# Kernel tuning notes

Hardware: AMD Instinct MI355X
Metric: run time of the kernel (lower is better)

Reference implementation:

```python
import jax, jax.numpy as jnp
from jax import lax
import numpy as np

SCALE, K_UP = 2, 5


def conv2d(x, w, pad=0, dil=1):
    return lax.conv_general_dilated(x, w, (1, 1), [(pad, pad), (pad, pad)],
                                    rhs_dilation=(dil, dil),
                                    dimension_numbers=('NCHW', 'OIHW', 'NCHW'))


def cbr(x, w, g, b, pad=0, relu=True):
    # Conv (no bias) + BatchNorm (eval: running_mean=0, running_var=1, eps=1e-5) + optional ReLU
    x = conv2d(x, w, pad)
    x = x * (g / jnp.sqrt(1.0 + 1e-5))[None, :, None, None] + b[None, :, None, None]
    return jnp.maximum(x, 0.0) if relu else x


def resize_bilinear_ac(x, ho, wo):
    # bilinear interpolation, align_corners=True (matches F.interpolate)
    B, C, H, W = x.shape
    ys = jnp.linspace(0.0, H - 1.0, ho)
    xs = jnp.linspace(0.0, W - 1.0, wo)
    y0 = jnp.floor(ys).astype(jnp.int32); y1 = jnp.minimum(y0 + 1, H - 1)
    x0 = jnp.floor(xs).astype(jnp.int32); x1 = jnp.minimum(x0 + 1, W - 1)
    wy = (ys - y0).astype(x.dtype)
    wx = (xs - x0).astype(x.dtype)
    top = x[:, :, y0, :]
    bot = x[:, :, y1, :]
    v = top * (1.0 - wy)[None, None, :, None] + bot * wy[None, None, :, None]
    return v[:, :, :, x0] * (1.0 - wx) + v[:, :, :, x1] * wx


def setup_inputs() -> dict:
    key = jax.random.key(0)
    ks = jax.random.split(key, 10)
    B, CH, CL, H, W = 4, 256, 128, 64, 64
    CMID, CO, IC, KENC = 64, 128, 64, 3

    def wgt(k, shape):
        fan = int(np.prod(shape[1:]))
        return (jax.random.normal(k, shape, jnp.float32) / np.sqrt(fan)).astype(jnp.float32)

    d = {}
    d['x_h'] = jax.random.normal(ks[0], (B, CH, H, W), jnp.float32)
    d['x_l'] = jax.random.normal(ks[1], (B, CL, H * SCALE, W * SCALE), jnp.float32)
    d['w_reduce'] = wgt(ks[2], (IC, CH, 3, 3)); d['g_reduce'] = jnp.ones(IC); d['b_reduce'] = jnp.zeros(IC)
    d['w1'] = wgt(ks[3], (CMID, CH, 1, 1)); d['g1'] = jnp.ones(CMID); d['b1'] = jnp.zeros(CMID)
    d['w2'] = wgt(ks[4], (CMID, CL, 1, 1)); d['g2'] = jnp.ones(CMID); d['b2'] = jnp.zeros(CMID)
    d['w_enc'] = wgt(ks[5], (K_UP * K_UP, 2 * CMID, KENC, KENC)); d['g_enc'] = jnp.ones(K_UP * K_UP); d['b_enc'] = jnp.zeros(K_UP * K_UP)
    d['w_out1'] = wgt(ks[6], (CO, IC + CL, 3, 3)); d['g_out1'] = jnp.ones(CO); d['b_out1'] = jnp.zeros(CO)
    d['w_out2'] = wgt(ks[7], (CO, CO, 1, 1)); d['g_out2'] = jnp.ones(CO); d['b_out2'] = jnp.zeros(CO)
    return d


def reference(x_h, x_l, w_reduce, g_reduce, b_reduce, w1, g1, b1, w2, g2, b2,
              w_enc, g_enc, b_enc, w_out1, g_out1, b_out1, w_out2, g_out2, b_out2):
    b, c, h, w = x_h.shape
    h_, w_ = h * SCALE, w * SCALE
    # content encoder -> per-pixel reassembly kernels
    x1 = resize_bilinear_ac(cbr(x_h, w1, g1, b1), h_, w_)          # [b, cmid, h_, w_]
    x2 = cbr(x_l, w2, g2, b2)                                       # [b, cmid, h_, w_]
    Wm = cbr(jnp.concatenate([x1, x2], axis=1), w_enc, g_enc, b_enc, pad=1, relu=False)
    Wm = jax.nn.softmax(Wm, axis=1)                                  # [b, k_up^2, h_, w_]
    # reduced high-level features, upsampled
    xr = cbr(x_h, w_reduce, g_reduce, b_reduce, pad=1)               # [b, ic, h, w]
    xu = resize_bilinear_ac(xr, h_, w_)                              # [b, ic, h_, w_]
    # CARAFE-style reassembly: unfold(k=5, dilation=2, pad=4) expressed as
    # 25 shifted windows of the zero-padded map -> no k^2-blown buffer.
    pad = (K_UP // 2) * SCALE
    xp = jnp.pad(xu, ((0, 0), (0, 0), (pad, pad), (pad, pad)))
    X = jnp.zeros_like(xu)
    for i in range(K_UP):
        for j in range(K_UP):
            win = xp[:, :, i * SCALE:i * SCALE + h_, j * SCALE:j * SCALE + w_]
            X = X + Wm[:, i * K_UP + j][:, None] * win
    y = jnp.concatenate([X, x_l], axis=1)
    y = cbr(y, w_out1, g_out1, b_out1, pad=1)
    y = cbr(y, w_out2, g_out2, b_out2)
    return y
```

## Files before the change

kernel.cpp:

```cpp
#include <hip/hip_runtime.h>
#include <math.h>

#define BNS 0.99999500003749981f

typedef short          bf16x8  __attribute__((ext_vector_type(8)));
typedef float          f32x4   __attribute__((ext_vector_type(4)));
typedef unsigned short u16x8   __attribute__((ext_vector_type(8)));
typedef unsigned short u16x4   __attribute__((ext_vector_type(4)));
typedef unsigned short ushort_t;

__device__ inline ushort_t f2b(float f) {
    union { float f; unsigned int u; } x; x.f = f;
    unsigned int u = x.u;
    unsigned int r = (u + 0x7FFFu + ((u >> 16) & 1u)) >> 16;
    return (ushort_t)r;
}
__device__ inline float b2f(ushort_t s) {
    union { unsigned int u; float f; } x; x.u = ((unsigned int)s) << 16;
    return x.f;
}

__device__ inline void glds16(const ushort_t* gp, void* lp) {
    __builtin_amdgcn_global_load_lds(
        (const __attribute__((address_space(1))) unsigned int*)gp,
        (__attribute__((address_space(3))) unsigned int*)lp, 16, 0, 0);
}

template<int N, bool LG0>
__device__ __forceinline__ void wait_v() {
    static_assert(N >= 0 && N <= 16, "vmcnt literal table");
    if constexpr (LG0) {
        if constexpr (N == 0)  asm volatile("s_waitcnt vmcnt(0) lgkmcnt(0)" ::: "memory");
        if constexpr (N == 3)  asm volatile("s_waitcnt vmcnt(3) lgkmcnt(0)" ::: "memory");
        if constexpr (N == 4)  asm volatile("s_waitcnt vmcnt(4) lgkmcnt(0)" ::: "memory");
        if constexpr (N == 6)  asm volatile("s_waitcnt vmcnt(6) lgkmcnt(0)" ::: "memory");
        if constexpr (N == 8)  asm volatile("s_waitcnt vmcnt(8) lgkmcnt(0)" ::: "memory");
    } else {
        if constexpr (N == 0)  asm volatile("s_waitcnt vmcnt(0)" ::: "memory");
        if constexpr (N == 3)  asm volatile("s_waitcnt vmcnt(3)" ::: "memory");
        if constexpr (N == 4)  asm volatile("s_waitcnt vmcnt(4)" ::: "memory");
        if constexpr (N == 6)  asm volatile("s_waitcnt vmcnt(6)" ::: "memory");
        if constexpr (N == 8)  asm volatile("s_waitcnt vmcnt(8)" ::: "memory");
    }
}

#define E_BWR   0u
#define E_BW1   147456u
#define E_BW2   163840u
#define E_BWE   172032u
#define E_BWO1  208896u
#define E_BWO2  430080u
#define E_ZP    446464u
#define OFF_R1  524288u
#define OFF_R4  4718592u
#define OFF_R2  8912896u
#define OFF_R3  9961472u
#define OFF_R6  11010048u
#define OFF_R5  13107200u


__device__ inline void wseg3(int idx, const float* src, ushort_t* dst,
                             int TAPS, int COT, int CIT, int CO_real) {
    int kt  = idx / (COT * 32);
    int r   = idx - kt * (COT * 32);
    int q   = r / (COT * 8);
    int r2  = r - q * (COT * 8);
    int co  = r2 >> 3;
    int e   = r2 & 7;
    int KCT = CIT >> 5;
    int tap = kt / KCT, j = kt - tap * KCT;
    int ci  = j * 32 + q * 8 + e;
    float v = (co < CO_real) ? src[((size_t)co * CIT + ci) * TAPS + tap] : 0.f;
    dst[idx] = f2b(v);
}

__device__ inline void cvt_t16(const float* __restrict__ in,
                               ushort_t* __restrict__ out,
                               int C, int LHW, int px, int npx) {
    if (px >= npx) return;
    int HW = 1 << LHW;
    int b = px >> LHW, phw = px & (HW - 1);
    const float* src = in + (size_t)b * C * HW + phw;
    unsigned base = (unsigned)(px >> 4) * (C * 16) + (unsigned)(px & 15) * 8;
    for (int c0 = 0; c0 < C; c0 += 8) {
        u16x8 o;
#pragma unroll
        for (int j = 0; j < 8; j++) o[j] = f2b(src[(size_t)(c0 + j) * HW]);
        *reinterpret_cast<u16x8*>(out + base + (c0 >> 3) * 128) = o;
    }
}

__global__ __launch_bounds__(256)
void prep_all(const float* wr, const float* w1, const float* w2,
              const float* we, const float* wo1, const float* wo2,
              const float* xh, const float* xl, ushort_t* ws0)
{
    int bx = blockIdx.x;
    int tid = threadIdx.x;
    if (bx < 1872) {
        int idx = bx * 256 + tid;
        const int n0 = 9*64*256;
        const int n1 = 64*256;
        const int n2 = 64*128;
        const int n3 = 9*32*128;
        const int n4 = 9*128*192;
        const int n5 = 128*128;
        if (idx < n0) { wseg3(idx, wr,  ws0 + E_BWR,  9, 64, 256, 64);  return; } idx -= n0;
        if (idx < n1) { wseg3(idx, w1,  ws0 + E_BW1,  1, 64, 256, 64);  return; } idx -= n1;
        if (idx < n2) { wseg3(idx, w2,  ws0 + E_BW2,  1, 64, 128, 64);  return; } idx -= n2;
        if (idx < n3) { wseg3(idx, we,  ws0 + E_BWE,  9, 32, 128, 25);  return; } idx -= n3;
        if (idx < n4) { wseg3(idx, wo1, ws0 + E_BWO1, 9, 128, 192, 128); return; } idx -= n4;
        if (idx < n5) { wseg3(idx, wo2, ws0 + E_BWO2, 1, 128, 128, 128); return; } idx -= n5;
        if (idx < 32768) ws0[E_ZP + idx] = 0;
        return;
    }
    bx -= 1872;
    if (bx < 64) { cvt_t16(xh, ws0 + OFF_R1, 256, 12, bx * 256 + tid, 16384); return; }
    bx -= 64;
    cvt_t16(xl, ws0 + OFF_R5, 128, 14, bx * 256 + tid, 65536);
}

template<int TAPS, int BM, int CIA, int CIB, int COT, int BN, int G,
         int WSX, int DEP, int EPI>
__global__ __launch_bounds__(256)
void conv_lds(const ushort_t* __restrict__ ws0,
              unsigned offA, unsigned offB, unsigned offW,
              const float* __restrict__ g, const float* __restrict__ bia,
              int COclamp, void* __restrict__ outp,
              int H, int LHW, int relu)
{
    constexpr int KCA = CIA / 32, KCB = CIB / 32;
    constexpr int KCT = KCA + KCB;
    constexpr int NW  = (TAPS == 9) ? 3 : G;
    constexpr int ACP = (TAPS == 9) ? 1 : G;
    constexpr int NPH = (TAPS == 9) ? 3 * KCT : KCT / G;
    constexpr int WSY = 4 / WSX;
    constexpr int MF = BM / WSX / 16;
    constexpr int NF = BN / WSY / 16;
    constexpr int ACHUNK = BM / 16;
    constexpr int A4 = (ACP * ACHUNK + 3) / 4;
    constexpr int WUNIT = BN / 16;
    constexpr int TWU = NW * WUNIT;
    constexpr int W4 = (TWU + 3) / 4;
    constexpr int SS = A4 + W4;
    constexpr int WOFF = ACP * BM * 64;
    constexpr int ZS   = WOFF + NW * BN * 64;
    constexpr int BUF  = ZS + 16;
    constexpr int LBN3 = (BN == 128) ? 10 : (BN == 64) ? 9 : 8;
    __shared__ __align__(16) char lds[DEP * BUF];

    const unsigned nx = gridDim.x, ox = blockIdx.x;
    const unsigned qq = nx >> 3, xcd = ox & 7, k0 = ox >> 3;
    const unsigned bx = xcd * qq + k0;
    const int co_blk = blockIdx.y * BN;

    const int tid = threadIdx.x, w = tid >> 6, lane = tid & 63;
    const int l15 = lane & 15, lhi = lane >> 4;
    const int wpx = (w % WSX) * (BM / WSX);
    const int cw0 = (w / WSX) * (BN / WSY);
    const int yb = (int)(bx & (unsigned)(H - 1));
    const unsigned pxc0 = bx * ACHUNK;

    if (tid < 4 * DEP) *(unsigned*)(lds + (tid >> 2) * BUF + ZS + (tid & 3) * 4) = 0u;

    int aA[3][MF];
#pragma unroll
    for (int dxi = 0; dxi < 3; ++dxi) {
        const int dx = dxi - 1;
#pragma unroll
        for (int mf = 0; mf < MF; ++mf) {
            int pr = wpx + mf * 16 + l15 + dx;
            bool ok = (TAPS == 1) ? true : (pr >= 0 && pr < BM);
            aA[dxi][mf] = ok ? (((pr >> 4) << 10) + (lhi << 8) + ((pr & 15) << 4)) : ZS;
        }
    }
    int wA[NF];
#pragma unroll
    for (int nf = 0; nf < NF; ++nf)
        wA[nf] = (lhi * BN + cw0 + nf * 16 + l15) * 16;

    f32x4 acc[NF][MF];
#pragma unroll
    for (int nf = 0; nf < NF; ++nf)
#pragma unroll
        for (int mf = 0; mf < MF; ++mf)
            acc[nf][mf] = (f32x4){0.f, 0.f, 0.f, 0.f};

    auto stage = [&](int p, int bsel) {
        char* lb = lds + bsel * BUF;
        if constexpr (TAPS == 9) {
            const int dyi = p / KCT, kc = p - dyi * KCT;
            const int dy = dyi - 1;
            const bool isA = (kc < KCA);
            const int kcs = isA ? kc : kc - KCA;
            const int CI  = isA ? CIA : CIB;
            const unsigned offS = isA ? offA : offB;
            const bool rowv = (yb + dy >= 0) && (yb + dy < H);
#pragma unroll
            for (int i = 0; i < A4; ++i) {
                int u = (i * 4 + w) % ACHUNK;
                unsigned s = rowv
                    ? offS + (unsigned)((int)pxc0 + dy * ACHUNK + u) * (unsigned)(CI * 16)
                           + (unsigned)(kcs * 512) + (unsigned)(lane * 8)
                    : E_ZP + (unsigned)(lane * 8);
                glds16(ws0 + s, lb + u * 1024);
            }
#pragma unroll
            for (int i = 0; i < W4; ++i) {
                int t3 = (i * 4 + w) % TWU;
                int tl = t3 / WUNIT, uu = t3 - tl * WUNIT;
                unsigned wsrc = offW + (unsigned)((dyi * 3 + tl) * KCT + kc)
                                       * (unsigned)(COT * 32);
                int el  = uu * 512 + lane * 8;
                int q   = el >> LBN3;
                int col = (el & ((1 << LBN3) - 1)) >> 3;
                glds16(ws0 + wsrc + q * (COT * 8) + (co_blk + col) * 8,
                       lb + WOFF + tl * (BN * 64) + uu * 1024);
            }
        } else {
#pragma unroll
            for (int i = 0; i < A4; ++i) {
                int lin = (i * 4 + w) % (ACP * ACHUNK);
                int gc = lin / ACHUNK, u = lin - gc * ACHUNK;
                unsigned s = offA + (unsigned)(pxc0 + u) * (unsigned)(CIA * 16)
                           + (unsigned)((p * G + gc) * 512) + (unsigned)(lane * 8);
                glds16(ws0 + s, lb + gc * (BM * 64) + u * 1024);
            }
#pragma unroll
            for (int i = 0; i < W4; ++i) {
                int t3 = (i * 4 + w) % TWU;
                int tl = t3 / WUNIT, uu = t3 - tl * WUNIT;
                unsigned wsrc = offW + (unsigned)(p * G + tl) * (unsigned)(COT * 32);
                int el  = uu * 512 + lane * 8;
                int q   = el >> LBN3;
                int col = (el & ((1 << LBN3) - 1)) >> 3;
                glds16(ws0 + wsrc + q * (COT * 8) + (co_blk + col) * 8,
                       lb + WOFF + tl * (BN * 64) + uu * 1024);
            }
        }
    };

    auto step = [&](int p, int bsel) {
        const char* lb = lds + bsel * BUF;
        __builtin_amdgcn_s_setprio(1);
#pragma unroll
        for (int t = 0; t < NW; ++t) {
            const int dxi = (TAPS == 9) ? t : 1;
            const char* ab = lb + ((TAPS == 9) ? 0 : t * (BM * 64));
            bf16x8 af[MF], wf[NF];
#pragma unroll
            for (int mf = 0; mf < MF; ++mf)
                af[mf] = *reinterpret_cast<const bf16x8*>(ab + aA[dxi][mf]);
#pragma unroll
            for (int nf = 0; nf < NF; ++nf)
                wf[nf] = *reinterpret_cast<const bf16x8*>(
                    lb + WOFF + t * (BN * 64) + wA[nf]);
#pragma unroll
            for (int nf = 0; nf < NF; ++nf)
#pragma unroll
                for (int mf = 0; mf < MF; ++mf)
                    acc[nf][mf] = __builtin_amdgcn_mfma_f32_16x16x32_bf16(
                        wf[nf], af[mf], acc[nf][mf], 0, 0, 0);
        }
        __builtin_amdgcn_s_setprio(0);
    };

    stage(0, 0);
    if constexpr (DEP == 3) { if (1 < NPH) stage(1, 1); }
#pragma unroll
    for (int p = 0; p < NPH; ++p) {
        if (p + DEP - 1 < NPH) stage(p + DEP - 1, (p + DEP - 1) % DEP);
        if constexpr (DEP == 3) {
            if (p == 0) {
                if (p + 2 < NPH)      wait_v<2 * SS, true >();
                else if (p + 1 < NPH) wait_v<SS,     true >();
                else                  wait_v<0,      true >();
            } else {
                if (p + 2 < NPH)      wait_v<2 * SS, false>();
                else if (p + 1 < NPH) wait_v<SS,     false>();
                else                  wait_v<0,      false>();
            }
        } else {
            if (p == 0) { if (p + 1 < NPH) wait_v<SS, true >(); else wait_v<0, true >(); }
            else        { if (p + 1 < NPH) wait_v<SS, false>(); else wait_v<0, false>(); }
        }
        __builtin_amdgcn_s_barrier();
        __builtin_amdgcn_sched_barrier(0);
        step(p, p % DEP);
        __builtin_amdgcn_sched_barrier(0);
        if (p + 1 < NPH) __builtin_amdgcn_s_barrier();
    }

    if constexpr (EPI == 0) {
        ushort_t* o1 = (ushort_t*)outp;
#pragma unroll
        for (int nf = 0; nf < NF; ++nf) {
            const int cg = co_blk + cw0 + nf * 16 + (lhi << 2);
            float sc[4], bi[4];
#pragma unroll
            for (int r = 0; r < 4; r++) {
                int c = min(cg + r, COclamp - 1);
                sc[r] = g[c] * BNS; bi[r] = bia[c];
            }
#pragma unroll
            for (int mf = 0; mf < MF; ++mf) {
                f32x4 a = acc[nf][mf];
                u16x4 ov;
#pragma unroll
                for (int r = 0; r < 4; r++) {
                    float v = fmaf(a[r], sc[r], bi[r]);
                    if (relu) v = fmaxf(v, 0.f);
                    ov[r] = f2b(v);
                }
                int px = (int)bx * BM + wpx + mf * 16 + l15;
                unsigned off = (unsigned)(px >> 4) * (COT * 16)
                             + (unsigned)(cg >> 3) * 128
                             + (unsigned)(px & 15) * 8 + (unsigned)(cg & 7);
                *reinterpret_cast<u16x4*>(o1 + off) = ov;
            }
        }
    } else if constexpr (EPI == 1) {
        float* o1 = (float*)outp;
        const int HW = 1 << LHW;
#pragma unroll
        for (int nf = 0; nf < NF; ++nf) {
            const int cg = co_blk + cw0 + nf * 16 + (lhi << 2);
            float sc[4], bi[4];
#pragma unroll
            for (int r = 0; r < 4; r++) {
                int c = min(cg + r, COclamp - 1);
                sc[r] = g[c] * BNS; bi[r] = bia[c];
            }
#pragma unroll
            for (int mf = 0; mf < MF; ++mf) {
                int px = (int)bx * BM + wpx + mf * 16 + l15;
                int b = px >> LHW, phw = px & (HW - 1);
#pragma unroll
                for (int r = 0; r < 4; r++) {
                    float v = fmaf(acc[nf][mf][r], sc[r], bi[r]);
                    if (relu) v = fmaxf(v, 0.f);
                    o1[((size_t)(b * COT + cg + r)) * HW + phw] = v;
                }
            }
        }
    } else {
        __syncthreads();
        float* sf = (float*)lds;
#pragma unroll
        for (int nf = 0; nf < NF; ++nf) {
            const int cg = cw0 + nf * 16 + (lhi << 2);
#pragma unroll
            for (int mf = 0; mf < MF; ++mf) {
                int pxl = wpx + mf * 16 + l15;
                f32x4 a = acc[nf][mf];
#pragma unroll
                for (int r = 0; r < 4; r++) {
                    int c = min(cg + r, COclamp - 1);
                    sf[(cg + r) * 136 + pxl] = fmaf(a[r], g[c] * BNS, bia[c]);
                }
            }
        }
        __syncthreads();
        if (tid < BM) {
            int gpx = (int)bx * BM + tid;
            float v[25];
#pragma unroll
            for (int c = 0; c < 25; ++c) v[c] = sf[c * 136 + tid];
            float m = v[0];
#pragma unroll
            for (int c = 1; c < 25; ++c) m = fmaxf(m, v[c]);
            float s = 0.f;
#pragma unroll
            for (int c = 0; c < 25; ++c) { v[c] = __expf(v[c] - m); s += v[c]; }
            float inv = 1.f / s;
            ushort_t* o1 = (ushort_t*)outp;
            unsigned base = (unsigned)(gpx >> 4) * (32 * 16) + (unsigned)(gpx & 15) * 8;
#pragma unroll
            for (int q = 0; q < 3; ++q) {
                u16x8 ov;
#pragma unroll
                for (int k = 0; k < 8; k++) ov[k] = f2b(v[q * 8 + k] * inv);
                *reinterpret_cast<u16x8*>(o1 + base + q * 128) = ov;
            }
            o1[base + 384] = f2b(v[24] * inv);
        }
    }
}

__global__ __launch_bounds__(256)
void resize2x_t16(const ushort_t* __restrict__ in, ushort_t* __restrict__ out)
{
    int t = blockIdx.x * 256 + threadIdx.x;
    int cg = t & 7;
    int opx = t >> 3;
    int xo = opx & 127;
    int rest = opx >> 7;
    int yo = rest & 127;
    int b  = rest >> 7;
    float fy = (float)yo * 63.f / 127.f;
    float fx = (float)xo * 63.f / 127.f;
    int y0 = (int)fy, x0 = (int)fx;
    float wy = fy - (float)y0, wx = fx - (float)x0;
    int y1 = min(y0 + 1, 63), x1 = min(x0 + 1, 63);
    int qb = b * 4096;
#define RD(Y, X) (*reinterpret_cast<const bf16x8*>(in + \
    (unsigned)(((qb + (Y) * 64 + (X)) >> 4) * 1024) + cg * 128 + ((qb + (Y) * 64 + (X)) & 15) * 8))
    bf16x8 v00 = RD(y0, x0), v01 = RD(y0, x1), v10 = RD(y1, x0), v11 = RD(y1, x1);
#undef RD
    u16x8 o;
#pragma unroll
    for (int k = 0; k < 8; k++) {
        float l = b2f((ushort_t)v00[k]) * (1.f - wy) + b2f((ushort_t)v10[k]) * wy;
        float r = b2f((ushort_t)v01[k]) * (1.f - wy) + b2f((ushort_t)v11[k]) * wy;
        o[k] = f2b(l * (1.f - wx) + r * wx);
    }
    *reinterpret_cast<u16x8*>(out + (unsigned)(opx >> 4) * 1024 + cg * 128 + (opx & 15) * 8) = o;
}

__global__ __launch_bounds__(256)
void carafe25(const ushort_t* __restrict__ wm, const ushort_t* __restrict__ xu,
              ushort_t* __restrict__ out)
{
    int t = blockIdx.x * 256 + threadIdx.x;
    int cg = t & 7;
    int px = t >> 3;
    int x = px & 127;
    int y = (px >> 7) & 127;
    const ushort_t* wp = wm + (unsigned)(px >> 4) * 512 + (px & 15) * 8;
    u16x8 r0 = *reinterpret_cast<const u16x8*>(wp);
    u16x8 r1 = *reinterpret_cast<const u16x8*>(wp + 128);
    u16x8 r2 = *reinterpret_cast<const u16x8*>(wp + 256);
    float v[25];
#pragma unroll
    for (int k = 0; k < 8; k++) v[k]      = b2f(r0[k]);
#pragma unroll
    for (int k = 0; k < 8; k++) v[8 + k]  = b2f(r1[k]);
#pragma unroll
    for (int k = 0; k < 8; k++) v[16 + k] = b2f(r2[k]);
    v[24] = b2f(wp[384]);

    float acc[8];
#pragma unroll
    for (int k = 0; k < 8; k++) acc[k] = 0.f;
#pragma unroll
    for (int i = 0; i < 5; i++) {
        int yy = y + 2 * i - 4;
#pragma unroll
        for (int j = 0; j < 5; j++) {
            int xx = x + 2 * j - 4;
            if (yy >= 0 && yy < 128 && xx >= 0 && xx < 128) {
                int q = px + (2 * i - 4) * 128 + (2 * j - 4);
                bf16x8 xv = *reinterpret_cast<const bf16x8*>(
                    xu + (unsigned)(q >> 4) * 1024 + cg * 128 + (q & 15) * 8);
                float wv = v[i * 5 + j];
#pragma unroll
                for (int k = 0; k < 8; k++)
                    acc[k] = fmaf(wv, b2f((ushort_t)xv[k]), acc[k]);
            }
        }
    }
    u16x8 o;
#pragma unroll
    for (int k = 0; k < 8; k++) o[k] = f2b(acc[k]);
    *reinterpret_cast<u16x8*>(out + (unsigned)(px >> 4) * 1024 + cg * 128 + (px & 15) * 8) = o;
}

extern "C" void kernel_launch(void* const* d_in, const int* in_sizes, int n_in,
                              void* d_out, int out_size, void* d_ws, size_t ws_size,
                              hipStream_t stream)
{
    const float* x_h      = (const float*)d_in[0];
    const float* x_l      = (const float*)d_in[1];
    const float* w_reduce = (const float*)d_in[2];
    const float* g_reduce = (const float*)d_in[3];
    const float* b_reduce = (const float*)d_in[4];
    const float* w1       = (const float*)d_in[5];
    const float* g1       = (const float*)d_in[6];
    const float* b1       = (const float*)d_in[7];
    const float* w2       = (const float*)d_in[8];
    const float* g2       = (const float*)d_in[9];
    const float* b2       = (const float*)d_in[10];
    const float* w_enc    = (const float*)d_in[11];
    const float* g_enc    = (const float*)d_in[12];
    const float* b_enc    = (const float*)d_in[13];
    const float* w_out1   = (const float*)d_in[14];
    const float* g_out1   = (const float*)d_in[15];
    const float* b_out1   = (const float*)d_in[16];
    const float* w_out2   = (const float*)d_in[17];
    const float* g_out2   = (const float*)d_in[18];
    const float* b_out2   = (const float*)d_in[19];

    ushort_t* ws0 = (ushort_t*)d_ws;

    const unsigned oXHC = OFF_R1;
    const unsigned oC1  = OFF_R2;
    const unsigned oXR  = OFF_R3;
    const unsigned oX1  = OFF_R4;
    const unsigned oXLC = OFF_R5;
    const unsigned oX2  = OFF_R1;
    const unsigned oWM  = OFF_R6;
    const unsigned oXU  = OFF_R4;
    const unsigned oXB  = OFF_R1;
    const unsigned oY1  = OFF_R4;

    prep_all<<<2192, 256, 0, stream>>>(w_reduce, w1, w2, w_enc, w_out1, w_out2,
                                       x_h, x_l, ws0);
    conv_lds<1, 64, 256, 0, 64, 64, 2, 2, 3, 0><<<dim3(256, 1), 256, 0, stream>>>(
        ws0, oXHC, 0u, E_BW1, g1, b1, 64, ws0 + oC1, 64, 12, 1);
    conv_lds<9, 64, 256, 0, 64, 64, 1, 2, 3, 0><<<dim3(256, 1), 256, 0, stream>>>(
        ws0, oXHC, 0u, E_BWR, g_reduce, b_reduce, 64, ws0 + oXR, 64, 12, 1);
    resize2x_t16<<<2048, 256, 0, stream>>>(ws0 + oC1, ws0 + oX1);
    conv_lds<1, 128, 128, 0, 64, 64, 1, 2, 3, 0><<<dim3(512, 1), 256, 0, stream>>>(
        ws0, oXLC, 0u, E_BW2, g2, b2, 64, ws0 + oX2, 128, 14, 1);
    conv_lds<9, 128, 64, 64, 32, 32, 1, 4, 3, 2><<<dim3(512, 1), 256, 0, stream>>>(
        ws0, oX1, oX2, E_BWE, g_enc, b_enc, 25, ws0 + oWM, 128, 14, 0);
    resize2x_t16<<<2048, 256, 0, stream>>>(ws0 + oXR, ws0 + oXU);
    carafe25<<<2048, 256, 0, stream>>>(ws0 + oWM, ws0 + oXU, ws0 + oXB);
    conv_lds<9, 128, 64, 128, 128, 128, 1, 2, 2, 0><<<dim3(512, 1), 256, 0, stream>>>(
        ws0, oXB, oXLC, E_BWO1, g_out1, b_out1, 128, ws0 + oY1, 128, 14, 1);
    conv_lds<1, 128, 128, 0, 128, 128, 2, 2, 2, 1><<<dim3(512, 1), 256, 0, stream>>>(
        ws0, oY1, 0u, E_BWO2, g_out2, b_out2, 128, d_out, 128, 14, 1);
}
```

Before: 135.6 us.

## Fuse 1x1 and 3x3 convs on x_h, stage final output through LDS

Adds a conv_dual kernel that computes the 3x3 reduce conv and the 1x1 conv1 on x_h in one pass. The 1x1 conv reuses the center-row activation tiles already staged for the 3x3 conv, so the input is read once and there is one fewer launch. The final 1x1 conv gets a new epilogue that writes fp32 output through LDS, giving coalesced 16-byte stores instead of scattered scalar ones. Wait counts become runtime values dispatched through a switch, which adds branches around the pipeline waits.

```diff
diff --git a/kernel.cpp b/kernel.cpp
--- a/kernel.cpp
+++ b/kernel.cpp
@@ -28,21 +28,44 @@
 
 template<int N, bool LG0>
 __device__ __forceinline__ void wait_v() {
-    static_assert(N >= 0 && N <= 16, "vmcnt literal table");
     if constexpr (LG0) {
         if constexpr (N == 0)  asm volatile("s_waitcnt vmcnt(0) lgkmcnt(0)" ::: "memory");
+        if constexpr (N == 2)  asm volatile("s_waitcnt vmcnt(2) lgkmcnt(0)" ::: "memory");
         if constexpr (N == 3)  asm volatile("s_waitcnt vmcnt(3) lgkmcnt(0)" ::: "memory");
         if constexpr (N == 4)  asm volatile("s_waitcnt vmcnt(4) lgkmcnt(0)" ::: "memory");
+        if constexpr (N == 5)  asm volatile("s_waitcnt vmcnt(5) lgkmcnt(0)" ::: "memory");
         if constexpr (N == 6)  asm volatile("s_waitcnt vmcnt(6) lgkmcnt(0)" ::: "memory");
         if constexpr (N == 8)  asm volatile("s_waitcnt vmcnt(8) lgkmcnt(0)" ::: "memory");
+        if constexpr (N == 9)  asm volatile("s_waitcnt vmcnt(9) lgkmcnt(0)" ::: "memory");
+        if constexpr (N == 10) asm volatile("s_waitcnt vmcnt(10) lgkmcnt(0)" ::: "memory");
+        if constexpr (N == 12) asm volatile("s_waitcnt vmcnt(12) lgkmcnt(0)" ::: "memory");
+        if constexpr (N == 16) asm volatile("s_waitcnt vmcnt(16) lgkmcnt(0)" ::: "memory");
     } else {
         if constexpr (N == 0)  asm volatile("s_waitcnt vmcnt(0)" ::: "memory");
+        if constexpr (N == 2)  asm volatile("s_waitcnt vmcnt(2)" ::: "memory");
         if constexpr (N == 3)  asm volatile("s_waitcnt vmcnt(3)" ::: "memory");
         if constexpr (N == 4)  asm volatile("s_waitcnt vmcnt(4)" ::: "memory");
+        if constexpr (N == 5)  asm volatile("s_waitcnt vmcnt(5)" ::: "memory");
         if constexpr (N == 6)  asm volatile("s_waitcnt vmcnt(6)" ::: "memory");
         if constexpr (N == 8)  asm volatile("s_waitcnt vmcnt(8)" ::: "memory");
-    }
-}
+        if constexpr (N == 9)  asm volatile("s_waitcnt vmcnt(9)" ::: "memory");
+        if constexpr (N == 10) asm volatile("s_waitcnt vmcnt(10)" ::: "memory");
+        if constexpr (N == 12) asm volatile("s_waitcnt vmcnt(12)" ::: "memory");
+        if constexpr (N == 16) asm volatile("s_waitcnt vmcnt(16)" ::: "memory");
+    }
+}
+#define WAITSW(nn, LG) do { switch (nn) {                       \
+    case 0:  wait_v<0,  LG>(); break;                           \
+    case 2:  wait_v<2,  LG>(); break;                           \
+    case 3:  wait_v<3,  LG>(); break;                           \
+    case 4:  wait_v<4,  LG>(); break;                           \
+    case 5:  wait_v<5,  LG>(); break;                           \
+    case 6:  wait_v<6,  LG>(); break;                           \
+    case 8:  wait_v<8,  LG>(); break;                           \
+    case 9:  wait_v<9,  LG>(); break;                           \
+    case 10: wait_v<10, LG>(); break;                           \
+    case 12: wait_v<12, LG>(); break;                           \
+    default: wait_v<16, LG>(); break; } } while (0)
 
 #define E_BWR   0u
 #define E_BW1   147456u
@@ -118,6 +141,161 @@
     if (bx < 64) { cvt_t16(xh, ws0 + OFF_R1, 256, 12, bx * 256 + tid, 16384); return; }
     bx -= 64;
     cvt_t16(xl, ws0 + OFF_R5, 128, 14, bx * 256 + tid, 65536);
+}
+
+__global__ __launch_bounds__(256)
+void conv_dual(const ushort_t* __restrict__ ws0,
+               unsigned offA, unsigned offWr, unsigned offW1,
+               const float* __restrict__ gR, const float* __restrict__ bR,
+               const float* __restrict__ g1, const float* __restrict__ b1,
+               ushort_t* __restrict__ outR, ushort_t* __restrict__ outC)
+{
+    constexpr int BM = 64, BN = 64, KCT = 8, DEP = 3, NPH = 24;
+    constexpr int MF = 2, NF = 2;
+    constexpr int WOFF = BM * 64;
+    constexpr int ZS   = WOFF + 4 * BN * 64;
+    constexpr int BUF  = ZS + 16;
+    __shared__ __align__(16) char lds[DEP * BUF];
+
+    const unsigned nx = gridDim.x, ox = blockIdx.x;
+    const unsigned qq = nx >> 3, xcd = ox & 7, k0 = ox >> 3;
+    const unsigned bx = xcd * qq + k0;
+
+    const int tid = threadIdx.x, w = tid >> 6, lane = tid & 63;
+    const int l15 = lane & 15, lhi = lane >> 4;
+    const int wpx = (w & 1) * 32, cw0 = (w >> 1) * 32;
+    const int yb = (int)(bx & 63u);
+    const unsigned pxc0 = bx * 4;
+
+    if (tid < 4 * DEP) *(unsigned*)(lds + (tid >> 2) * BUF + ZS + (tid & 3) * 4) = 0u;
+
+    int aA[3][MF];
+#pragma unroll
+    for (int dxi = 0; dxi < 3; ++dxi)
+#pragma unroll
+        for (int mf = 0; mf < MF; ++mf) {
+            int pr = wpx + mf * 16 + l15 + dxi - 1;
+            bool ok = (pr >= 0) && (pr < BM);
+            aA[dxi][mf] = ok ? (((pr >> 4) << 10) + (lhi << 8) + ((pr & 15) << 4)) : ZS;
+        }
+    int wA[NF];
+#pragma unroll
+    for (int nf = 0; nf < NF; ++nf)
+        wA[nf] = lhi * 1024 + (cw0 + nf * 16 + l15) * 16;
+
+    f32x4 acc[NF][MF], acc2[NF][MF];
+#pragma unroll
+    for (int nf = 0; nf < NF; ++nf)
+#pragma unroll
+        for (int mf = 0; mf < MF; ++mf) {
+            acc[nf][mf]  = (f32x4){0.f, 0.f, 0.f, 0.f};
+            acc2[nf][mf] = (f32x4){0.f, 0.f, 0.f, 0.f};
+        }
+
+    auto stage = [&](int p, int bsel) {
+        char* lb = lds + bsel * BUF;
+        const int dyi = p >> 3, kc = p & 7;
+        const int dy = dyi - 1;
+        const bool rowv = (yb + dy >= 0) && (yb + dy < 64);
+        unsigned s = rowv
+            ? offA + (unsigned)((int)pxc0 + dy * 4 + w) * 4096u
+                   + (unsigned)(kc * 512) + (unsigned)(lane * 8)
+            : E_ZP + (unsigned)(lane * 8);
+        glds16(ws0 + s, lb + w * 1024);
+#pragma unroll
+        for (int i = 0; i < 3; ++i) {
+            int t3 = i * 4 + w;
+            int tl = t3 >> 2, uu = t3 & 3;
+            unsigned wsrc = offWr + (unsigned)(((dyi * 3 + tl) * KCT + kc) * 2048)
+                          + (unsigned)(uu * 512) + (unsigned)(lane * 8);
+            glds16(ws0 + wsrc, lb + WOFF + tl * 4096 + uu * 1024);
+        }
+        if (dyi == 1) {
+            unsigned wsrc = offW1 + (unsigned)(kc * 2048)
+                          + (unsigned)(w * 512) + (unsigned)(lane * 8);
+            glds16(ws0 + wsrc, lb + WOFF + 3 * 4096 + w * 1024);
+        }
+    };
+
+    auto step = [&](int p, int bsel) {
+        const char* lb = lds + bsel * BUF;
+        const int dyi = p >> 3;
+        __builtin_amdgcn_s_setprio(1);
+#pragma unroll
+        for (int t = 0; t < 3; ++t) {
+            bf16x8 af[MF], wf[NF];
+#pragma unroll
+            for (int mf = 0; mf < MF; ++mf)
+                af[mf] = *reinterpret_cast<const bf16x8*>(lb + aA[t][mf]);
+#pragma unroll
+            for (int nf = 0; nf < NF; ++nf)
+                wf[nf] = *reinterpret_cast<const bf16x8*>(lb + WOFF + t * 4096 + wA[nf]);
+#pragma unroll
+            for (int nf = 0; nf < NF; ++nf)
+#pragma unroll
+                for (int mf = 0; mf < MF; ++mf)
+                    acc[nf][mf] = __builtin_amdgcn_mfma_f32_16x16x32_bf16(
+                        wf[nf], af[mf], acc[nf][mf], 0, 0, 0);
+        }
+        if (dyi == 1) {
+            bf16x8 af[MF], wf[NF];
+#pragma unroll
+            for (int mf = 0; mf < MF; ++mf)
+                af[mf] = *reinterpret_cast<const bf16x8*>(lb + aA[1][mf]);
+#pragma unroll
+            for (int nf = 0; nf < NF; ++nf)
+                wf[nf] = *reinterpret_cast<const bf16x8*>(lb + WOFF + 3 * 4096 + wA[nf]);
+#pragma unroll
+            for (int nf = 0; nf < NF; ++nf)
+#pragma unroll
+                for (int mf = 0; mf < MF; ++mf)
+                    acc2[nf][mf] = __builtin_amdgcn_mfma_f32_16x16x32_bf16(
+                        wf[nf], af[mf], acc2[nf][mf], 0, 0, 0);
+        }
+        __builtin_amdgcn_s_setprio(0);
+    };
+
+    stage(0, 0); stage(1, 1);
+#pragma unroll
+    for (int p = 0; p < NPH; ++p) {
+        if (p + 2 < NPH) stage(p + 2, (p + 2) % 3);
+        int n1 = (p + 1 < NPH) ? ((((p + 1) >> 3) == 1) ? 5 : 4) : 0;
+        int n2 = (p + 2 < NPH) ? ((((p + 2) >> 3) == 1) ? 5 : 4) : 0;
+        int nn = n1 + n2;
+        if (p == 0) WAITSW(nn, true); else WAITSW(nn, false);
+        __builtin_amdgcn_s_barrier();
+        __builtin_amdgcn_sched_barrier(0);
+        step(p, p % 3);
+        __builtin_amdgcn_sched_barrier(0);
+        if (p + 1 < NPH) __builtin_amdgcn_s_barrier();
+    }
+
+#pragma unroll
+    for (int which = 0; which < 2; ++which) {
+        const float* gg = which ? g1 : gR;
+        const float* bb = which ? b1 : bR;
+        ushort_t* oo = which ? outC : outR;
+#pragma unroll
+        for (int nf = 0; nf < NF; ++nf) {
+            const int cg = cw0 + nf * 16 + (lhi << 2);
+            float sc[4], bi[4];
+#pragma unroll
+            for (int r = 0; r < 4; r++) { sc[r] = gg[cg + r] * BNS; bi[r] = bb[cg + r]; }
+#pragma unroll
+            for (int mf = 0; mf < MF; ++mf) {
+                f32x4 a = which ? acc2[nf][mf] : acc[nf][mf];
+                u16x4 ov;
+#pragma unroll
+                for (int r = 0; r < 4; r++)
+                    ov[r] = f2b(fmaxf(fmaf(a[r], sc[r], bi[r]), 0.f));
+                int px = (int)bx * BM + wpx + mf * 16 + l15;
+                unsigned off = (unsigned)(px >> 4) * 1024
+                             + (unsigned)(cg >> 3) * 128
+                             + (unsigned)(px & 15) * 8 + (unsigned)(cg & 7);
+                *reinterpret_cast<u16x4*>(oo + off) = ov;
+            }
+        }
+    }
 }
 
 template<int TAPS, int BM, int CIA, int CIB, int COT, int BN, int G,
@@ -270,20 +448,9 @@
 #pragma unroll
     for (int p = 0; p < NPH; ++p) {
         if (p + DEP - 1 < NPH) stage(p + DEP - 1, (p + DEP - 1) % DEP);
-        if constexpr (DEP == 3) {
-            if (p == 0) {
-                if (p + 2 < NPH)      wait_v<2 * SS, true >();
-                else if (p + 1 < NPH) wait_v<SS,     true >();
-                else                  wait_v<0,      true >();
-            } else {
-                if (p + 2 < NPH)      wait_v<2 * SS, false>();
-                else if (p + 1 < NPH) wait_v<SS,     false>();
-                else                  wait_v<0,      false>();
-            }
-        } else {
-            if (p == 0) { if (p + 1 < NPH) wait_v<SS, true >(); else wait_v<0, true >(); }
-            else        { if (p + 1 < NPH) wait_v<SS, false>(); else wait_v<0, false>(); }
-        }
+        int rem = NPH - 1 - p;
+        int nn = (rem >= DEP - 1 ? DEP - 1 : rem) * SS;
+        if (p == 0) WAITSW(nn, true); else WAITSW(nn, false);
         __builtin_amdgcn_s_barrier();
         __builtin_amdgcn_sched_barrier(0);
         step(p, p % DEP);
@@ -343,7 +510,7 @@
                 }
             }
         }
-    } else {
+    } else if constexpr (EPI == 2) {
         __syncthreads();
         float* sf = (float*)lds;
 #pragma unroll
@@ -383,6 +550,46 @@
                 *reinterpret_cast<u16x8*>(o1 + base + q * 128) = ov;
             }
             o1[base + 384] = f2b(v[24] * inv);
+        }
+    } else {
+        float* o1 = (float*)outp;
+        float* sf = (float*)lds;
+        const int phw_base = (int)((bx & 127u) * 128);
+        const int bimg = (int)(bx >> 7);
+        const int lane32 = tid & 31, cog = tid >> 5;
+#pragma unroll
+        for (int c = 0; c < 2; ++c) {
+            __syncthreads();
+            if (cw0 == c * 64) {
+#pragma unroll
+                for (int nf = 0; nf < NF; ++nf) {
+                    const int cgl = nf * 16 + (lhi << 2);
+                    const int cg  = c * 64 + cgl;
+                    float sc[4], bi[4];
+#pragma unroll
+                    for (int r = 0; r < 4; r++) { sc[r] = g[cg + r] * BNS; bi[r] = bia[cg + r]; }
+#pragma unroll
+                    for (int mf = 0; mf < MF; ++mf) {
+                        int pxl = wpx + mf * 16 + l15;
+                        f32x4 a = acc[nf][mf];
+#pragma unroll
+                        for (int r = 0; r < 4; r++) {
+                            float v = fmaf(a[r], sc[r], bi[r]);
+                            if (relu) v = fmaxf(v, 0.f);
+                            sf[(cgl + r) * 132 + pxl] = v;
+                        }
+                    }
+                }
+            }
+            __syncthreads();
+#pragma unroll
+            for (int j = 0; j < 8; ++j) {
+                int col = cog + j * 8;
+                f32x4 v = *reinterpret_cast<const f32x4*>(sf + col * 132 + lane32 * 4);
+                *reinterpret_cast<f32x4*>(
+                    o1 + (((size_t)bimg * 128 + c * 64 + col) << 14)
+                       + phw_base + lane32 * 4) = v;
+            }
         }
     }
 }
@@ -505,10 +712,9 @@
 
     prep_all<<<2192, 256, 0, stream>>>(w_reduce, w1, w2, w_enc, w_out1, w_out2,
                                        x_h, x_l, ws0);
-    conv_lds<1, 64, 256, 0, 64, 64, 2, 2, 3, 0><<<dim3(256, 1), 256, 0, stream>>>(
-        ws0, oXHC, 0u, E_BW1, g1, b1, 64, ws0 + oC1, 64, 12, 1);
-    conv_lds<9, 64, 256, 0, 64, 64, 1, 2, 3, 0><<<dim3(256, 1), 256, 0, stream>>>(
-        ws0, oXHC, 0u, E_BWR, g_reduce, b_reduce, 64, ws0 + oXR, 64, 12, 1);
+    conv_dual<<<256, 256, 0, stream>>>(
+        ws0, oXHC, E_BWR, E_BW1, g_reduce, b_reduce, g1, b1,
+        ws0 + oXR, ws0 + oC1);
     resize2x_t16<<<2048, 256, 0, stream>>>(ws0 + oC1, ws0 + oX1);
     conv_lds<1, 128, 128, 0, 64, 64, 1, 2, 3, 0><<<dim3(512, 1), 256, 0, stream>>>(
         ws0, oXLC, 0u, E_BW2, g2, b2, 64, ws0 + oX2, 128, 14, 1);
@@ -518,6 +724,6 @@
     carafe25<<<2048, 256, 0, stream>>>(ws0 + oWM, ws0 + oXU, ws0 + oXB);
     conv_lds<9, 128, 64, 128, 128, 128, 1, 2, 2, 0><<<dim3(512, 1), 256, 0, stream>>>(
         ws0, oXB, oXLC, E_BWO1, g_out1, b_out1, 128, ws0 + oY1, 128, 14, 1);
-    conv_lds<1, 128, 128, 0, 128, 128, 2, 2, 2, 1><<<dim3(512, 1), 256, 0, stream>>>(
+    conv_lds<1, 128, 128, 0, 128, 128, 2, 2, 2, 3><<<dim3(512, 1), 256, 0, stream>>>(
         ws0, oY1, 0u, E_BWO2, g_out2, b_out2, 128, d_out, 128, 14, 1);
 }
```

Measured after the change: 133.9 us. Within noise of the previous version (-1.2%).
